# Performance work log

Hardware: AMD Instinct MI355X
Metric: run time of the kernel (lower is better)

The kernel has to match this reference:

```python
import jax, jax.numpy as jnp
import numpy as np


def setup_inputs() -> dict:
    key = jax.random.key(0)
    k1, k2 = jax.random.split(key)
    B, S_ENC, S_DEC, D = 8, 2048, 2048, 1024
    enc_outputs = jax.random.normal(k1, (B, S_ENC, D), dtype=jnp.float32)
    dec_outputs = jax.random.normal(k2, (B, S_DEC, D), dtype=jnp.float32)
    return {"enc_outputs": enc_outputs, "dec_outputs": dec_outputs}


def reference(enc_outputs, dec_outputs):
    # scores: [B, S_enc, S_dec] = enc @ dec^T (unscaled)
    a_t = jnp.einsum('bed,btd->bet', enc_outputs, dec_outputs)
    a_t = jax.nn.softmax(a_t, axis=-1)
    # context: [B, S_dec, D] = a_t^T @ enc
    c_t = jnp.einsum('bet,bed->btd', a_t, enc_outputs)
    return c_t
```

## Files before the change

kernel.cpp:

```cpp
#include <hip/hip_runtime.h>


typedef _Float16 half8 __attribute__((ext_vector_type(8)));
typedef _Float16 half4v __attribute__((ext_vector_type(4)));
typedef float floatx16 __attribute__((ext_vector_type(16)));

#define BM 128
#define BN 128
#define BK 64

__device__ __forceinline__ void async_load16(const _Float16* g, void* l) {
  __builtin_amdgcn_global_load_lds(
      (const __attribute__((address_space(1))) void*)g,
      (__attribute__((address_space(3))) void*)l, 16, 0, 0);
}

template <typename OutT, bool TRANS, int RN>
__global__ __launch_bounds__(256, 2) void gemm_bt(
    const _Float16* __restrict__ A, const _Float16* __restrict__ Bt,
    OutT* __restrict__ C, int K, long strideA, long strideB, long strideC,
    int ldA, int ldB, int ldC) {
  constexpr int CPR = BK / 8;
  constexpr int SK = BK / 16;
  __shared__ alignas(16) char smem[TRANS ? (128 * 136 * 2) : (2 * BM * BK * 2)];
  _Float16* lds_a = (_Float16*)smem;
  _Float16* lds_b = (_Float16*)(smem + BM * BK * 2);

  const int b = blockIdx.z;
  A += (long)b * strideA;
  Bt += (long)b * strideB;
  C += (long)b * strideC;

  const int id = blockIdx.y * gridDim.x + blockIdx.x;
  const int xcd = id & 7;
  const int l = id >> 3;
  const int m0 = ((xcd & 3) * 4 + l / RN) * BM;
  const int n0 = ((xcd >> 2) * RN + l % RN) * BN;

  const int tid = threadIdx.x;
  const int lane = tid & 63;
  const int wave = tid >> 6;
  const int l31 = lane & 31;
  const int kh = lane >> 5;
  const int wm = (wave >> 1) * 64;
  const int wn = (wave & 1) * 64;

  floatx16 acc[2][2] = {};

  for (int k0 = 0; k0 < K; k0 += BK) {
#pragma unroll
    for (int c = 0; c < 4; ++c) {
      const int off = c * 4096 + wave * 1024 + lane * 16;
      const int row = off >> 7;
      const int ke = (((off >> 4) & (CPR - 1)) ^ (row & (CPR - 1))) * 8;
      async_load16(A + (long)(m0 + row) * ldA + k0 + ke, (char*)lds_a + off);
      async_load16(Bt + (long)(n0 + row) * ldB + k0 + ke, (char*)lds_b + off);
    }
    __syncthreads();

    half8 af[2][SK], bf[2][SK];
#pragma unroll
    for (int i = 0; i < 2; ++i) {
      const int ra = wm + i * 32 + l31;
      const int rb = wn + i * 32 + l31;
#pragma unroll
      for (int s = 0; s < SK; ++s) {
        const int ck = s * 2 + kh;
        af[i][s] = *(const half8*)((const char*)lds_a + ra * (BK * 2) +
                                   ((ck ^ (ra & (CPR - 1))) << 4));
        bf[i][s] = *(const half8*)((const char*)lds_b + rb * (BK * 2) +
                                   ((ck ^ (rb & (CPR - 1))) << 4));
      }
    }
#pragma unroll
    for (int s = 0; s < SK; ++s)
#pragma unroll
      for (int i = 0; i < 2; ++i)
#pragma unroll
        for (int j = 0; j < 2; ++j)
          acc[i][j] = __builtin_amdgcn_mfma_f32_32x32x16_f16(
              af[i][s], bf[j][s], acc[i][j], 0, 0, 0);
    __syncthreads();
  }

  if constexpr (TRANS) {
    _Float16(*TT)[136] = (_Float16(*)[136])smem;
#pragma unroll
    for (int i = 0; i < 2; ++i)
#pragma unroll
      for (int j = 0; j < 2; ++j) {
        const int tl = wn + j * 32 + l31;
#pragma unroll
        for (int g = 0; g < 4; ++g) {
          half4v h;
#pragma unroll
          for (int rr = 0; rr < 4; ++rr) h[rr] = (_Float16)acc[i][j][g * 4 + rr];
          *(half4v*)&TT[tl][wm + i * 32 + 4 * kh + g * 8] = h;
        }
      }
    __syncthreads();
#pragma unroll
    for (int p = 0; p < 8; ++p) {
      const int idx = p * 256 + tid;
      const int tl = idx >> 4;
      const int ck = idx & 15;
      *(half8*)((_Float16*)C + (long)(n0 + tl) * ldC + m0 + ck * 8) =
          *(const half8*)&TT[tl][ck * 8];
    }
  } else {
#pragma unroll
    for (int i = 0; i < 2; ++i) {
      const int r_base = m0 + wm + i * 32 + 4 * kh;
#pragma unroll
      for (int j = 0; j < 2; ++j) {
        const int col = n0 + wn + j * 32 + l31;
#pragma unroll
        for (int g = 0; g < 4; ++g)
#pragma unroll
          for (int rr = 0; rr < 4; ++rr)
            C[(long)(r_base + g * 8 + rr) * ldC + col] =
                (OutT)acc[i][j][g * 4 + rr];
      }
    }
  }
}

__global__ __launch_bounds__(256) void conv_enc(const float* __restrict__ E,
                                                _Float16* __restrict__ Eh,
                                                _Float16* __restrict__ EhT,
                                                int Se, int D) {
  __shared__ _Float16 T[64][72];
  const int b = blockIdx.z;
  const int d0 = blockIdx.x * 64;
  const int e0 = blockIdx.y * 64;
  const float* Eb = E + (size_t)b * Se * D;
  _Float16* Ehb = Eh + (size_t)b * Se * D;
  _Float16* EhTb = EhT + (size_t)b * D * Se;
  const int tid = threadIdx.x;
  const int tx = tid & 15;
  const int ty = tid >> 4;

  half4v h[4];
#pragma unroll
  for (int r = 0; r < 4; ++r) {
    const int e = e0 + ty * 4 + r;
    float4 v = *(const float4*)(Eb + (size_t)e * D + d0 + tx * 4);
    h[r][0] = (_Float16)v.x; h[r][1] = (_Float16)v.y;
    h[r][2] = (_Float16)v.z; h[r][3] = (_Float16)v.w;
    *(half4v*)(Ehb + (size_t)e * D + d0 + tx * 4) = h[r];
  }
#pragma unroll
  for (int c = 0; c < 4; ++c) {
    half4v w;
#pragma unroll
    for (int r = 0; r < 4; ++r) w[r] = h[r][c];
    *(half4v*)&T[tx * 4 + c][ty * 4] = w;
  }
  __syncthreads();
#pragma unroll
  for (int p = 0; p < 2; ++p) {
    const int idx = tid + p * 256;
    const int row = idx >> 3;
    const int ck = idx & 7;
    *(half8*)(EhTb + (size_t)(d0 + row) * Se + e0 + ck * 8) =
        *(const half8*)&T[row][ck * 8];
  }
}

__global__ __launch_bounds__(256) void conv_dec(const float* __restrict__ X,
                                                _Float16* __restrict__ Y) {
  const size_t i = ((size_t)blockIdx.x * 256 + threadIdx.x) * 8;
  float4 a = *(const float4*)(X + i);
  float4 b = *(const float4*)(X + i + 4);
  half8 h;
  h[0] = (_Float16)a.x; h[1] = (_Float16)a.y;
  h[2] = (_Float16)a.z; h[3] = (_Float16)a.w;
  h[4] = (_Float16)b.x; h[5] = (_Float16)b.y;
  h[6] = (_Float16)b.z; h[7] = (_Float16)b.w;
  *(half8*)(Y + i) = h;
}

__global__ __launch_bounds__(256) void col_stats(const _Float16* __restrict__ ST,
                                                 float2* __restrict__ part) {
  __shared__ float2 red[16][65];
  const int b = blockIdx.z;
  const int e0 = blockIdx.x * 64;
  const int t0 = blockIdx.y * 512;
  const _Float16* S = ST + (size_t)b * 2048 * 2048;
  const int tx = threadIdx.x & 15;
  const int ty = threadIdx.x >> 4;

  float m[4] = {-1e30f, -1e30f, -1e30f, -1e30f};
  float s[4] = {0.f, 0.f, 0.f, 0.f};
  for (int it = 0; it < 32; ++it) {
    const int t = t0 + it * 16 + ty;
    half4v v = *(const half4v*)(S + (size_t)t * 2048 + e0 + tx * 4);
#pragma unroll
    for (int c = 0; c < 4; ++c) {
      const float x = (float)v[c];
      const float m2 = fmaxf(m[c], x);
      s[c] = s[c] * __expf(m[c] - m2) + __expf(x - m2);
      m[c] = m2;
    }
  }
#pragma unroll
  for (int c = 0; c < 4; ++c) red[ty][tx * 4 + c] = make_float2(m[c], s[c]);
  __syncthreads();
  if (threadIdx.x < 64) {
    float2 a = red[0][threadIdx.x];
#pragma unroll
    for (int r = 1; r < 16; ++r) {
      const float2 o = red[r][threadIdx.x];
      const float m2 = fmaxf(a.x, o.x);
      a.y = a.y * __expf(a.x - m2) + o.y * __expf(o.x - m2);
      a.x = m2;
    }
    part[(size_t)blockIdx.y * 16384 + (size_t)b * 2048 + e0 + threadIdx.x] = a;
  }
}

__global__ __launch_bounds__(256) void stats_combine(
    const float2* __restrict__ part, float2* __restrict__ stats) {
  const int idx = blockIdx.x * 256 + threadIdx.x;
  float2 a = part[idx];
#pragma unroll
  for (int tc = 1; tc < 4; ++tc) {
    const float2 o = part[tc * 16384 + idx];
    const float m2 = fmaxf(a.x, o.x);
    a.y = a.y * __expf(a.x - m2) + o.y * __expf(o.x - m2);
    a.x = m2;
  }
  stats[idx] = make_float2(a.x, 1.0f / a.y);
}

__global__ __launch_bounds__(256) void norm_stream(
    const _Float16* __restrict__ ST, const float2* __restrict__ stats,
    _Float16* __restrict__ P) {
  const int b = blockIdx.y;
  const int t0 = blockIdx.x * 4;
  const int e = threadIdx.x * 8;
  float m_[8], rl_[8];
#pragma unroll
  for (int j = 0; j < 8; ++j) {
    const float2 st = stats[(size_t)b * 2048 + e + j];
    m_[j] = st.x;
    rl_[j] = st.y;
  }
  const size_t base = ((size_t)b * 2048 + t0) * 2048 + e;
#pragma unroll
  for (int r = 0; r < 4; ++r) {
    half8 v = *(const half8*)(ST + base + (size_t)r * 2048);
    half8 o;
#pragma unroll
    for (int j = 0; j < 8; ++j)
      o[j] = (_Float16)(__expf((float)v[j] - m_[j]) * rl_[j]);
    *(half8*)(P + base + (size_t)r * 2048) = o;
  }
}

extern "C" void kernel_launch(void* const* d_in, const int* in_sizes, int n_in,
                              void* d_out, int out_size, void* d_ws,
                              size_t ws_size, hipStream_t stream) {
  const float* enc = (const float*)d_in[0];
  const float* dec = (const float*)d_in[1];
  float* out = (float*)d_out;

  const int B = 8, SE = 2048, SD = 2048, D = 1024;
  char* ws = (char*)d_ws;
  _Float16* enc_h = (_Float16*)ws;
  _Float16* dec_h = (_Float16*)(ws + 33554432);
  _Float16* P = (_Float16*)ws;
  _Float16* enc_hT = (_Float16*)(ws + 67108864);
  _Float16* ST = (_Float16*)(ws + 100663296);
  float2* stats = (float2*)(ws + 167772160);
  float2* part = (float2*)(ws + 167903232);

  conv_enc<<<dim3(D / 64, SE / 64, B), 256, 0, stream>>>(enc, enc_h, enc_hT,
                                                         SE, D);
  conv_dec<<<dim3((size_t)B * SD * D / 2048), 256, 0, stream>>>(dec, dec_h);
  gemm_bt<_Float16, true, 8><<<dim3(SD / BN, SE / BM, B), 256, 0, stream>>>(
      enc_h, dec_h, ST, D, (long)SE * D, (long)SD * D, (long)SE * SD, D, D,
      SE);
  col_stats<<<dim3(32, 4, B), 256, 0, stream>>>(ST, part);
  stats_combine<<<dim3(64), 256, 0, stream>>>(part, stats);
  norm_stream<<<dim3(512, B), 256, 0, stream>>>(ST, stats, P);
  gemm_bt<float, false, 4><<<dim3(D / BN, SD / BM, B), 256, 0, stream>>>(
      P, enc_hT, out, SE, (long)SD * SE, (long)D * SE, (long)SD * D, SE, SE,
      D);
}
```

Before: 349.9 us.

## Fuse softmax column stats into score GEMM and normalization into context GEMM

The score GEMM epilogue now computes per-tile column max and sum from the transposed LDS tile and writes partial stats, which removes the separate col_stats pass over the score matrix. The context GEMM applies exp2(x*log2e - q) while loading its A operand, with q folding the max and log-sum, so the norm_stream pass that read and wrote the full probability matrix is gone. The A operand of the second GEMM is now a synchronous global load plus conversion instead of an async global-to-LDS copy, and exps are recomputed once per N-tile (8 times per element). Launch bounds also rise to 4 blocks per CU.

New measurement: 423.7 us. +21.1%, slower.

```diff
diff --git a/kernel.cpp b/kernel.cpp
--- a/kernel.cpp
+++ b/kernel.cpp
@@ -1,4 +1,5 @@
 #include <hip/hip_runtime.h>
+#include <math.h>
 
 
 typedef _Float16 half8 __attribute__((ext_vector_type(8)));
@@ -8,6 +9,7 @@
 #define BM 128
 #define BN 128
 #define BK 64
+#define LOG2E 1.44269504088896340736f
 
 __device__ __forceinline__ void async_load16(const _Float16* g, void* l) {
   __builtin_amdgcn_global_load_lds(
@@ -15,14 +17,16 @@
       (__attribute__((address_space(3))) void*)l, 16, 0, 0);
 }
 
-template <typename OutT, bool TRANS, int RN>
-__global__ __launch_bounds__(256, 2) void gemm_bt(
+template <typename OutT, bool TRANS, bool NORM, int RN>
+__global__ __launch_bounds__(256, 4) void gemm_bt(
     const _Float16* __restrict__ A, const _Float16* __restrict__ Bt,
-    OutT* __restrict__ C, int K, long strideA, long strideB, long strideC,
+    OutT* __restrict__ C, const float* __restrict__ qv,
+    float2* __restrict__ part, int K, long strideA, long strideB, long strideC,
     int ldA, int ldB, int ldC) {
   constexpr int CPR = BK / 8;
   constexpr int SK = BK / 16;
   __shared__ alignas(16) char smem[TRANS ? (128 * 136 * 2) : (2 * BM * BK * 2)];
+  __shared__ float2 cred[256];
   _Float16* lds_a = (_Float16*)smem;
   _Float16* lds_b = (_Float16*)(smem + BM * BK * 2);
 
@@ -30,6 +34,7 @@
   A += (long)b * strideA;
   Bt += (long)b * strideB;
   C += (long)b * strideC;
+  const float* qb = qv ? qv + (long)b * 2048 : nullptr;
 
   const int id = blockIdx.y * gridDim.x + blockIdx.x;
   const int xcd = id & 7;
@@ -53,7 +58,19 @@
       const int off = c * 4096 + wave * 1024 + lane * 16;
       const int row = off >> 7;
       const int ke = (((off >> 4) & (CPR - 1)) ^ (row & (CPR - 1))) * 8;
-      async_load16(A + (long)(m0 + row) * ldA + k0 + ke, (char*)lds_a + off);
+      if constexpr (NORM) {
+        half8 v = *(const half8*)(A + (long)(m0 + row) * ldA + k0 + ke);
+        float4 q0 = *(const float4*)(qb + k0 + ke);
+        float4 q1 = *(const float4*)(qb + k0 + ke + 4);
+        float qf[8] = {q0.x, q0.y, q0.z, q0.w, q1.x, q1.y, q1.z, q1.w};
+        half8 o;
+#pragma unroll
+        for (int j = 0; j < 8; ++j)
+          o[j] = (_Float16)exp2f((float)v[j] * LOG2E - qf[j]);
+        *(half8*)((char*)lds_a + off) = o;
+      } else {
+        async_load16(A + (long)(m0 + row) * ldA + k0 + ke, (char*)lds_a + off);
+      }
       async_load16(Bt + (long)(n0 + row) * ldB + k0 + ke, (char*)lds_b + off);
     }
     __syncthreads();
@@ -106,6 +123,28 @@
       const int ck = idx & 15;
       *(half8*)((_Float16*)C + (long)(n0 + tl) * ldC + m0 + ck * 8) =
           *(const half8*)&TT[tl][ck * 8];
+    }
+    {
+      const int e_l = tid & 127;
+      const int th = tid >> 7;
+      float m = -1e30f, s = 0.f;
+#pragma unroll 8
+      for (int t = th * 64; t < th * 64 + 64; ++t) {
+        const float x = (float)TT[t][e_l];
+        const float m2 = fmaxf(m, x);
+        s = s * __expf(m - m2) + __expf(x - m2);
+        m = m2;
+      }
+      cred[tid] = make_float2(m, s);
+      __syncthreads();
+      if (tid < 128) {
+        const float2 a = cred[tid];
+        const float2 o = cred[tid + 128];
+        const float m2 = fmaxf(a.x, o.x);
+        const float ss = a.y * __expf(a.x - m2) + o.y * __expf(o.x - m2);
+        part[((long)(n0 >> 7) * 8 + b) * 2048 + m0 + tid] =
+            make_float2(m2, ss);
+      }
     }
   } else {
 #pragma unroll
@@ -180,82 +219,20 @@
   *(half8*)(Y + i) = h;
 }
 
-__global__ __launch_bounds__(256) void col_stats(const _Float16* __restrict__ ST,
-                                                 float2* __restrict__ part) {
-  __shared__ float2 red[16][65];
-  const int b = blockIdx.z;
-  const int e0 = blockIdx.x * 64;
-  const int t0 = blockIdx.y * 512;
-  const _Float16* S = ST + (size_t)b * 2048 * 2048;
-  const int tx = threadIdx.x & 15;
-  const int ty = threadIdx.x >> 4;
-
-  float m[4] = {-1e30f, -1e30f, -1e30f, -1e30f};
-  float s[4] = {0.f, 0.f, 0.f, 0.f};
-  for (int it = 0; it < 32; ++it) {
-    const int t = t0 + it * 16 + ty;
-    half4v v = *(const half4v*)(S + (size_t)t * 2048 + e0 + tx * 4);
-#pragma unroll
-    for (int c = 0; c < 4; ++c) {
-      const float x = (float)v[c];
-      const float m2 = fmaxf(m[c], x);
-      s[c] = s[c] * __expf(m[c] - m2) + __expf(x - m2);
-      m[c] = m2;
-    }
-  }
-#pragma unroll
-  for (int c = 0; c < 4; ++c) red[ty][tx * 4 + c] = make_float2(m[c], s[c]);
-  __syncthreads();
-  if (threadIdx.x < 64) {
-    float2 a = red[0][threadIdx.x];
-#pragma unroll
-    for (int r = 1; r < 16; ++r) {
-      const float2 o = red[r][threadIdx.x];
-      const float m2 = fmaxf(a.x, o.x);
-      a.y = a.y * __expf(a.x - m2) + o.y * __expf(o.x - m2);
-      a.x = m2;
-    }
-    part[(size_t)blockIdx.y * 16384 + (size_t)b * 2048 + e0 + threadIdx.x] = a;
-  }
-}
-
 __global__ __launch_bounds__(256) void stats_combine(
-    const float2* __restrict__ part, float2* __restrict__ stats) {
+    const float2* __restrict__ part, float* __restrict__ q) {
   const int idx = blockIdx.x * 256 + threadIdx.x;
-  float2 a = part[idx];
-#pragma unroll
-  for (int tc = 1; tc < 4; ++tc) {
-    const float2 o = part[tc * 16384 + idx];
+  const int b = idx >> 11;
+  const int e = idx & 2047;
+  float2 a = part[(long)b * 2048 + e];
+#pragma unroll
+  for (int tb = 1; tb < 16; ++tb) {
+    const float2 o = part[((long)tb * 8 + b) * 2048 + e];
     const float m2 = fmaxf(a.x, o.x);
     a.y = a.y * __expf(a.x - m2) + o.y * __expf(o.x - m2);
     a.x = m2;
   }
-  stats[idx] = make_float2(a.x, 1.0f / a.y);
-}
-
-__global__ __launch_bounds__(256) void norm_stream(
-    const _Float16* __restrict__ ST, const float2* __restrict__ stats,
-    _Float16* __restrict__ P) {
-  const int b = blockIdx.y;
-  const int t0 = blockIdx.x * 4;
-  const int e = threadIdx.x * 8;
-  float m_[8], rl_[8];
-#pragma unroll
-  for (int j = 0; j < 8; ++j) {
-    const float2 st = stats[(size_t)b * 2048 + e + j];
-    m_[j] = st.x;
-    rl_[j] = st.y;
-  }
-  const size_t base = ((size_t)b * 2048 + t0) * 2048 + e;
-#pragma unroll
-  for (int r = 0; r < 4; ++r) {
-    half8 v = *(const half8*)(ST + base + (size_t)r * 2048);
-    half8 o;
-#pragma unroll
-    for (int j = 0; j < 8; ++j)
-      o[j] = (_Float16)(__expf((float)v[j] - m_[j]) * rl_[j]);
-    *(half8*)(P + base + (size_t)r * 2048) = o;
-  }
+  q[idx] = a.x * LOG2E + log2f(a.y);
 }
 
 extern "C" void kernel_launch(void* const* d_in, const int* in_sizes, int n_in,
@@ -269,22 +246,21 @@
   char* ws = (char*)d_ws;
   _Float16* enc_h = (_Float16*)ws;
   _Float16* dec_h = (_Float16*)(ws + 33554432);
-  _Float16* P = (_Float16*)ws;
   _Float16* enc_hT = (_Float16*)(ws + 67108864);
   _Float16* ST = (_Float16*)(ws + 100663296);
-  float2* stats = (float2*)(ws + 167772160);
-  float2* part = (float2*)(ws + 167903232);
+  float* q = (float*)(ws + 167772160);
+  float2* part = (float2*)(ws + 167837696);
 
   conv_enc<<<dim3(D / 64, SE / 64, B), 256, 0, stream>>>(enc, enc_h, enc_hT,
                                                          SE, D);
   conv_dec<<<dim3((size_t)B * SD * D / 2048), 256, 0, stream>>>(dec, dec_h);
-  gemm_bt<_Float16, true, 8><<<dim3(SD / BN, SE / BM, B), 256, 0, stream>>>(
-      enc_h, dec_h, ST, D, (long)SE * D, (long)SD * D, (long)SE * SD, D, D,
-      SE);
-  col_stats<<<dim3(32, 4, B), 256, 0, stream>>>(ST, part);
-  stats_combine<<<dim3(64), 256, 0, stream>>>(part, stats);
-  norm_stream<<<dim3(512, B), 256, 0, stream>>>(ST, stats, P);
-  gemm_bt<float, false, 4><<<dim3(D / BN, SD / BM, B), 256, 0, stream>>>(
-      P, enc_hT, out, SE, (long)SD * SE, (long)D * SE, (long)SD * D, SE, SE,
-      D);
-}
+  gemm_bt<_Float16, true, false, 8>
+      <<<dim3(SD / BN, SE / BM, B), 256, 0, stream>>>(
+          enc_h, dec_h, ST, nullptr, part, D, (long)SE * D, (long)SD * D,
+          (long)SE * SD, D, D, SE);
+  stats_combine<<<dim3(64), 256, 0, stream>>>(part, q);
+  gemm_bt<float, false, true, 4>
+      <<<dim3(D / BN, SD / BM, B), 256, 0, stream>>>(
+          ST, enc_hT, out, q, nullptr, SE, (long)SD * SE, (long)D * SE,
+          (long)SD * D, SE, SE, D);
+}
```
